# Optimization experiments

Measured on AMD Instinct MI355X. Metric: run time of the kernel, lower is better.

The kernel has to match this reference:

```python
import jax, jax.numpy as jnp
import numpy as np

EMBED_DIM = 1024
NUM_HEADS = 16
HEAD_DIM = EMBED_DIM // NUM_HEADS
B, S = 4, 1024


def setup_inputs() -> dict:
    key = jax.random.key(0)
    kq, kk, kw, kb, kd = jax.random.split(key, 5)
    q = jax.random.normal(kq, (B, NUM_HEADS, S, HEAD_DIM), dtype=jnp.float32)
    k = jax.random.normal(kk, (B, NUM_HEADS, S, HEAD_DIM), dtype=jnp.float32)
    # nn.Bilinear(out_features=1) weight per head is [1, D, D]; stacked -> [H, D, D]
    W = jax.random.normal(kw, (NUM_HEADS, HEAD_DIM, HEAD_DIM), dtype=jnp.float32) * (1.0 / np.sqrt(HEAD_DIM))
    b = jax.random.normal(kb, (NUM_HEADS,), dtype=jnp.float32) * 0.02
    Wd = jnp.full((NUM_HEADS,), 0.5, dtype=jnp.float32)  # init tt.tensor(0.5)
    return {"q": q, "k": k, "W": W, "b": b, "Wd": Wd}


def reference(q, k, W, b, Wd):
    scale = EMBED_DIM ** 0.5
    # raw scaled logits: note original multiplies by sqrt(embed_dim)
    d = jnp.einsum("bhid,bhjd->bhij", q, k) * scale
    # per-pair bilinear score: q_i^T W_h k_j + b_h, gated by Wd_h
    bil = jnp.einsum("bhid,hde,bhje->bhij", q, W, k)
    d = d + (bil + b[None, :, None, None]) * Wd[None, :, None, None]
    return d
```

## Files before the change

kernel.cpp:

```cpp
#include <hip/hip_runtime.h>
#include <hip/hip_bf16.h>

#define S_LEN 1024
#define HD 64
#define NBH 64

typedef __attribute__((ext_vector_type(8))) short short8;
typedef __attribute__((ext_vector_type(4))) float floatx4;

__device__ __forceinline__ unsigned short f2bf(float f) {
  unsigned int u = __builtin_bit_cast(unsigned int, f);
  u += 0x7fffu + ((u >> 16) & 1u);
  return (unsigned short)(u >> 16);
}

__global__ __launch_bounds__(256) void prep_small_kernel(
    const float* __restrict__ W, const float* __restrict__ Wd,
    unsigned short* __restrict__ MT) {
  int idx = blockIdx.x * 256 + threadIdx.x;
  int h  = idx >> 12;
  int n  = (idx >> 6) & 63;
  int kk = idx & 63;
  float v = Wd[h] * W[(h << 12) + (kk << 6) + n];
  if (kk == n) v += 32.0f;
  MT[idx] = f2bf(v);
}

__global__ __launch_bounds__(256) void prep_q_kernel(
    const float* __restrict__ q, const unsigned short* __restrict__ MT,
    unsigned short* __restrict__ qp) {
  const int bh   = blockIdx.y;
  const int h    = bh & 15;
  const int wave = threadIdx.x >> 6;
  const int lane = threadIdx.x & 63;
  const int l15  = lane & 15;
  const int quad = lane >> 4;
  const int i0   = blockIdx.x * 256 + wave * 64;

  const float* __restrict__ qb = q + (size_t)bh * S_LEN * HD;
  const unsigned short* __restrict__ mt = MT + (h << 12);

  short8 bfrag[4][2];
#pragma unroll
  for (int nt = 0; nt < 4; nt++)
#pragma unroll
    for (int ks = 0; ks < 2; ks++)
      bfrag[nt][ks] = *(const short8*)(mt + (nt * 16 + l15) * HD + ks * 32 + quad * 8);

  short8 afrag[4][2];
#pragma unroll
  for (int mtile = 0; mtile < 4; mtile++)
#pragma unroll
    for (int ks = 0; ks < 2; ks++) {
      const float* src = qb + (size_t)(i0 + mtile * 16 + l15) * HD + ks * 32 + quad * 8;
      floatx4 a0 = *(const floatx4*)src;
      floatx4 a1 = *(const floatx4*)(src + 4);
      short8 f;
      f[0] = f2bf(a0[0]); f[1] = f2bf(a0[1]); f[2] = f2bf(a0[2]); f[3] = f2bf(a0[3]);
      f[4] = f2bf(a1[0]); f[5] = f2bf(a1[1]); f[6] = f2bf(a1[2]); f[7] = f2bf(a1[3]);
      afrag[mtile][ks] = f;
    }

  floatx4 acc[4][4];
#pragma unroll
  for (int mtile = 0; mtile < 4; mtile++)
#pragma unroll
    for (int nt = 0; nt < 4; nt++) {
      acc[mtile][nt] = (floatx4){0.f, 0.f, 0.f, 0.f};
#pragma unroll
      for (int ks = 0; ks < 2; ks++)
        acc[mtile][nt] = __builtin_amdgcn_mfma_f32_16x16x32_bf16(
            afrag[mtile][ks], bfrag[nt][ks], acc[mtile][nt], 0, 0, 0);
    }

  unsigned short* __restrict__ qpb = qp + (size_t)bh * S_LEN * HD;
#pragma unroll
  for (int mtile = 0; mtile < 4; mtile++)
#pragma unroll
    for (int nt = 0; nt < 4; nt++)
#pragma unroll
      for (int r = 0; r < 4; r++) {
        int row = i0 + mtile * 16 + quad * 4 + r;
        int col = nt * 16 + l15;
        qpb[row * HD + col] = f2bf(acc[mtile][nt][r]);
      }
}

__global__ __launch_bounds__(256) void main_kernel(
    const unsigned short* __restrict__ qp, const float* __restrict__ kmat,
    const float* __restrict__ b, const float* __restrict__ Wd,
    float* __restrict__ out) {
  const int bh   = blockIdx.z;
  const int h    = bh & 15;
  const int wave = threadIdx.x >> 6;
  const int lane = threadIdx.x & 63;
  const int l15  = lane & 15;
  const int quad = lane >> 4;
  const int row0 = blockIdx.y * 128 + (wave >> 1) * 64;
  const int col0 = blockIdx.x * 128 + (wave & 1) * 64;

  const unsigned short* __restrict__ qb = qp + (size_t)bh * S_LEN * HD;
  const float* __restrict__ kb = kmat + (size_t)bh * S_LEN * HD;

  short8 afrag[4][2];
#pragma unroll
  for (int mtile = 0; mtile < 4; mtile++)
#pragma unroll
    for (int ks = 0; ks < 2; ks++)
      afrag[mtile][ks] =
          *(const short8*)(qb + (row0 + mtile * 16 + l15) * HD + ks * 32 + quad * 8);

  short8 bfrag[4][2];
#pragma unroll
  for (int nt = 0; nt < 4; nt++)
#pragma unroll
    for (int ks = 0; ks < 2; ks++) {
      const float* src = kb + (size_t)(col0 + nt * 16 + l15) * HD + ks * 32 + quad * 8;
      floatx4 a0 = *(const floatx4*)src;
      floatx4 a1 = *(const floatx4*)(src + 4);
      short8 f;
      f[0] = f2bf(a0[0]); f[1] = f2bf(a0[1]); f[2] = f2bf(a0[2]); f[3] = f2bf(a0[3]);
      f[4] = f2bf(a1[0]); f[5] = f2bf(a1[1]); f[6] = f2bf(a1[2]); f[7] = f2bf(a1[3]);
      bfrag[nt][ks] = f;
    }

  floatx4 acc[4][4];
#pragma unroll
  for (int mtile = 0; mtile < 4; mtile++)
#pragma unroll
    for (int nt = 0; nt < 4; nt++) {
      acc[mtile][nt] = (floatx4){0.f, 0.f, 0.f, 0.f};
#pragma unroll
      for (int ks = 0; ks < 2; ks++)
        acc[mtile][nt] = __builtin_amdgcn_mfma_f32_16x16x32_bf16(
            afrag[mtile][ks], bfrag[nt][ks], acc[mtile][nt], 0, 0, 0);
    }

  const float cbias = Wd[h] * b[h];
  float* __restrict__ ob = out + (size_t)bh * S_LEN * S_LEN;
#pragma unroll
  for (int mtile = 0; mtile < 4; mtile++)
#pragma unroll
    for (int r = 0; r < 4; r++) {
      int row = row0 + mtile * 16 + quad * 4 + r;
      float* orow = ob + (size_t)row * S_LEN + col0;
#pragma unroll
      for (int nt = 0; nt < 4; nt++)
        __builtin_nontemporal_store(acc[mtile][nt][r] + cbias, orow + nt * 16 + l15);
    }
}

extern "C" void kernel_launch(void* const* d_in, const int* in_sizes, int n_in,
                              void* d_out, int out_size, void* d_ws, size_t ws_size,
                              hipStream_t stream) {
  const float* q  = (const float*)d_in[0];
  const float* k  = (const float*)d_in[1];
  const float* W  = (const float*)d_in[2];
  const float* b  = (const float*)d_in[3];
  const float* Wd = (const float*)d_in[4];
  float* out = (float*)d_out;

  unsigned short* qp = (unsigned short*)d_ws;
  unsigned short* MT = qp + (size_t)NBH * S_LEN * HD;

  prep_small_kernel<<<256, 256, 0, stream>>>(W, Wd, MT);
  prep_q_kernel<<<dim3(4, NBH), 256, 0, stream>>>(q, MT, qp);
  main_kernel<<<dim3(8, 8, NBH), 256, 0, stream>>>(qp, k, b, Wd, out);
}
```

Before: 332.2 us.

## Pre-convert K to bf16, stage output via LDS for vector stores, shrink q-prep tiles

Adds a separate kernel that converts K to bf16 once, so the main kernel no longer re-reads fp32 K and re-converts it in each of the eight row blocks. The main kernel folds the bias into the accumulator init and stages results through padded per-wave LDS so each lane writes 16-byte contiguous nontemporal stores instead of scalar strided ones. prep_q uses 16-row tiles per wave to launch more blocks. This costs an extra launch and a bf16 K workspace write and read, plus LDS use that may limit occupancy.

```diff
diff --git a/kernel.cpp b/kernel.cpp
--- a/kernel.cpp
+++ b/kernel.cpp
@@ -1,5 +1,4 @@
 #include <hip/hip_runtime.h>
-#include <hip/hip_bf16.h>
 
 #define S_LEN 1024
 #define HD 64
@@ -7,6 +6,7 @@
 
 typedef __attribute__((ext_vector_type(8))) short short8;
 typedef __attribute__((ext_vector_type(4))) float floatx4;
+typedef __attribute__((ext_vector_type(4))) unsigned short ushort4v;
 
 __device__ __forceinline__ unsigned short f2bf(float f) {
   unsigned int u = __builtin_bit_cast(unsigned int, f);
@@ -26,6 +26,15 @@
   MT[idx] = f2bf(v);
 }
 
+__global__ __launch_bounds__(256) void convert_k_kernel(
+    const float* __restrict__ k, unsigned short* __restrict__ kp) {
+  size_t t = (size_t)blockIdx.x * 256 + threadIdx.x;
+  floatx4 v = *(const floatx4*)(k + t * 4);
+  ushort4v o;
+  o[0] = f2bf(v[0]); o[1] = f2bf(v[1]); o[2] = f2bf(v[2]); o[3] = f2bf(v[3]);
+  *(ushort4v*)(kp + t * 4) = o;
+}
+
 __global__ __launch_bounds__(256) void prep_q_kernel(
     const float* __restrict__ q, const unsigned short* __restrict__ MT,
     unsigned short* __restrict__ qp) {
@@ -35,7 +44,7 @@
   const int lane = threadIdx.x & 63;
   const int l15  = lane & 15;
   const int quad = lane >> 4;
-  const int i0   = blockIdx.x * 256 + wave * 64;
+  const int i0   = blockIdx.x * 64 + wave * 16;
 
   const float* __restrict__ qb = q + (size_t)bh * S_LEN * HD;
   const unsigned short* __restrict__ mt = MT + (h << 12);
@@ -47,49 +56,43 @@
     for (int ks = 0; ks < 2; ks++)
       bfrag[nt][ks] = *(const short8*)(mt + (nt * 16 + l15) * HD + ks * 32 + quad * 8);
 
-  short8 afrag[4][2];
+  short8 afrag[2];
 #pragma unroll
-  for (int mtile = 0; mtile < 4; mtile++)
+  for (int ks = 0; ks < 2; ks++) {
+    const float* src = qb + (size_t)(i0 + l15) * HD + ks * 32 + quad * 8;
+    floatx4 a0 = *(const floatx4*)src;
+    floatx4 a1 = *(const floatx4*)(src + 4);
+    short8 f;
+    f[0] = f2bf(a0[0]); f[1] = f2bf(a0[1]); f[2] = f2bf(a0[2]); f[3] = f2bf(a0[3]);
+    f[4] = f2bf(a1[0]); f[5] = f2bf(a1[1]); f[6] = f2bf(a1[2]); f[7] = f2bf(a1[3]);
+    afrag[ks] = f;
+  }
+
+  floatx4 acc[4];
 #pragma unroll
-    for (int ks = 0; ks < 2; ks++) {
-      const float* src = qb + (size_t)(i0 + mtile * 16 + l15) * HD + ks * 32 + quad * 8;
-      floatx4 a0 = *(const floatx4*)src;
-      floatx4 a1 = *(const floatx4*)(src + 4);
-      short8 f;
-      f[0] = f2bf(a0[0]); f[1] = f2bf(a0[1]); f[2] = f2bf(a0[2]); f[3] = f2bf(a0[3]);
-      f[4] = f2bf(a1[0]); f[5] = f2bf(a1[1]); f[6] = f2bf(a1[2]); f[7] = f2bf(a1[3]);
-      afrag[mtile][ks] = f;
-    }
-
-  floatx4 acc[4][4];
+  for (int nt = 0; nt < 4; nt++) {
+    acc[nt] = (floatx4){0.f, 0.f, 0.f, 0.f};
 #pragma unroll
-  for (int mtile = 0; mtile < 4; mtile++)
-#pragma unroll
-    for (int nt = 0; nt < 4; nt++) {
-      acc[mtile][nt] = (floatx4){0.f, 0.f, 0.f, 0.f};
-#pragma unroll
-      for (int ks = 0; ks < 2; ks++)
-        acc[mtile][nt] = __builtin_amdgcn_mfma_f32_16x16x32_bf16(
-            afrag[mtile][ks], bfrag[nt][ks], acc[mtile][nt], 0, 0, 0);
-    }
+    for (int ks = 0; ks < 2; ks++)
+      acc[nt] = __builtin_amdgcn_mfma_f32_16x16x32_bf16(afrag[ks], bfrag[nt][ks],
+                                                        acc[nt], 0, 0, 0);
+  }
 
   unsigned short* __restrict__ qpb = qp + (size_t)bh * S_LEN * HD;
 #pragma unroll
-  for (int mtile = 0; mtile < 4; mtile++)
+  for (int nt = 0; nt < 4; nt++)
 #pragma unroll
-    for (int nt = 0; nt < 4; nt++)
-#pragma unroll
-      for (int r = 0; r < 4; r++) {
-        int row = i0 + mtile * 16 + quad * 4 + r;
-        int col = nt * 16 + l15;
-        qpb[row * HD + col] = f2bf(acc[mtile][nt][r]);
-      }
+    for (int r = 0; r < 4; r++)
+      qpb[(i0 + quad * 4 + r) * HD + nt * 16 + l15] = f2bf(acc[nt][r]);
 }
 
+#define LPAD 68
 __global__ __launch_bounds__(256) void main_kernel(
-    const unsigned short* __restrict__ qp, const float* __restrict__ kmat,
+    const unsigned short* __restrict__ qp, const unsigned short* __restrict__ kp,
     const float* __restrict__ b, const float* __restrict__ Wd,
     float* __restrict__ out) {
+  __shared__ __align__(16) float lds[4 * 32 * LPAD];
+
   const int bh   = blockIdx.z;
   const int h    = bh & 15;
   const int wave = threadIdx.x >> 6;
@@ -99,55 +102,54 @@
   const int row0 = blockIdx.y * 128 + (wave >> 1) * 64;
   const int col0 = blockIdx.x * 128 + (wave & 1) * 64;
 
-  const unsigned short* __restrict__ qb = qp + (size_t)bh * S_LEN * HD;
-  const float* __restrict__ kb = kmat + (size_t)bh * S_LEN * HD;
+  const unsigned short* __restrict__ qb = qp + ((size_t)bh << 16);
+  const unsigned short* __restrict__ kb = kp + ((size_t)bh << 16);
 
-  short8 afrag[4][2];
+  short8 afrag[4][2], bfrag[4][2];
 #pragma unroll
-  for (int mtile = 0; mtile < 4; mtile++)
-#pragma unroll
-    for (int ks = 0; ks < 2; ks++)
-      afrag[mtile][ks] =
-          *(const short8*)(qb + (row0 + mtile * 16 + l15) * HD + ks * 32 + quad * 8);
-
-  short8 bfrag[4][2];
-#pragma unroll
-  for (int nt = 0; nt < 4; nt++)
+  for (int t = 0; t < 4; t++)
 #pragma unroll
     for (int ks = 0; ks < 2; ks++) {
-      const float* src = kb + (size_t)(col0 + nt * 16 + l15) * HD + ks * 32 + quad * 8;
-      floatx4 a0 = *(const floatx4*)src;
-      floatx4 a1 = *(const floatx4*)(src + 4);
-      short8 f;
-      f[0] = f2bf(a0[0]); f[1] = f2bf(a0[1]); f[2] = f2bf(a0[2]); f[3] = f2bf(a0[3]);
-      f[4] = f2bf(a1[0]); f[5] = f2bf(a1[1]); f[6] = f2bf(a1[2]); f[7] = f2bf(a1[3]);
-      bfrag[nt][ks] = f;
+      afrag[t][ks] = *(const short8*)(qb + (row0 + t * 16 + l15) * HD + ks * 32 + quad * 8);
+      bfrag[t][ks] = *(const short8*)(kb + (col0 + t * 16 + l15) * HD + ks * 32 + quad * 8);
     }
 
+  const float cbias = Wd[h] * b[h];
   floatx4 acc[4][4];
 #pragma unroll
   for (int mtile = 0; mtile < 4; mtile++)
 #pragma unroll
     for (int nt = 0; nt < 4; nt++) {
-      acc[mtile][nt] = (floatx4){0.f, 0.f, 0.f, 0.f};
+      acc[mtile][nt] = (floatx4){cbias, cbias, cbias, cbias};
 #pragma unroll
       for (int ks = 0; ks < 2; ks++)
         acc[mtile][nt] = __builtin_amdgcn_mfma_f32_16x16x32_bf16(
             afrag[mtile][ks], bfrag[nt][ks], acc[mtile][nt], 0, 0, 0);
     }
 
-  const float cbias = Wd[h] * b[h];
-  float* __restrict__ ob = out + (size_t)bh * S_LEN * S_LEN;
+  float* __restrict__ wlds = lds + wave * (32 * LPAD);
+  float* __restrict__ ob = out + ((size_t)bh << 20);
 #pragma unroll
-  for (int mtile = 0; mtile < 4; mtile++)
+  for (int c = 0; c < 2; ++c) {
 #pragma unroll
-    for (int r = 0; r < 4; r++) {
-      int row = row0 + mtile * 16 + quad * 4 + r;
-      float* orow = ob + (size_t)row * S_LEN + col0;
+    for (int mr = 0; mr < 2; ++mr) {
+      int mtile = 2 * c + mr;
 #pragma unroll
       for (int nt = 0; nt < 4; nt++)
-        __builtin_nontemporal_store(acc[mtile][nt][r] + cbias, orow + nt * 16 + l15);
+#pragma unroll
+        for (int r = 0; r < 4; r++)
+          wlds[(mr * 16 + quad * 4 + r) * LPAD + nt * 16 + l15] = acc[mtile][nt][r];
     }
+    __asm__ volatile("s_waitcnt lgkmcnt(0)" ::: "memory");
+#pragma unroll
+    for (int g = 0; g < 8; ++g) {
+      int row = g * 4 + quad;
+      floatx4 v = *(const floatx4*)(wlds + row * LPAD + l15 * 4);
+      __builtin_nontemporal_store(
+          v, (floatx4*)(ob + (size_t)(row0 + c * 32 + row) * S_LEN + col0 + l15 * 4));
+    }
+    __asm__ volatile("s_waitcnt lgkmcnt(0)" ::: "memory");
+  }
 }
 
 extern "C" void kernel_launch(void* const* d_in, const int* in_sizes, int n_in,
@@ -161,9 +163,11 @@
   float* out = (float*)d_out;
 
   unsigned short* qp = (unsigned short*)d_ws;
-  unsigned short* MT = qp + (size_t)NBH * S_LEN * HD;
+  unsigned short* kp = qp + (size_t)NBH * S_LEN * HD;
+  unsigned short* MT = kp + (size_t)NBH * S_LEN * HD;
 
   prep_small_kernel<<<256, 256, 0, stream>>>(W, Wd, MT);
-  prep_q_kernel<<<dim3(4, NBH), 256, 0, stream>>>(q, MT, qp);
-  main_kernel<<<dim3(8, 8, NBH), 256, 0, stream>>>(qp, k, b, Wd, out);
+  convert_k_kernel<<<4096, 256, 0, stream>>>(k, kp);
+  prep_q_kernel<<<dim3(16, NBH), 256, 0, stream>>>(q, MT, qp);
+  main_kernel<<<dim3(8, 8, NBH), 256, 0, stream>>>(qp, kp, b, Wd, out);
 }
```

Result: faster. 306.8 us (-7.7%).
